# Kernel tuning notes

Measured on AMD Instinct MI355X. Metric: run time of the kernel, lower is better.

The kernel has to match this reference:

```python
import jax, jax.numpy as jnp
import numpy as np
import math

B, L, M, D, EL, H = 128, 105, 55, 256, 3, 1
PATCH = [3, 5, 7]

def pos_embed(T, d):
    pos = jnp.arange(T, dtype=jnp.float32)[:, None]
    div = jnp.exp(jnp.arange(0, d, 2, dtype=jnp.float32) * (-math.log(10000.0) / d))
    pe = jnp.zeros((T, d), dtype=jnp.float32)
    pe = pe.at[:, 0::2].set(jnp.sin(pos * div))
    pe = pe.at[:, 1::2].set(jnp.cos(pos * div))
    return pe

def circular_conv(x, w):
    # x: [N, T, Cin], w: [Dout, Cin, 3]; Conv1d kernel 3, circular padding 1, no bias
    xc = jnp.pad(x.transpose(0, 2, 1), ((0, 0), (0, 0), (1, 1)), mode='wrap')
    y = jax.lax.conv_general_dilated(xc, w, (1,), 'VALID', dimension_numbers=('NCH', 'OIH', 'NCH'))
    return y.transpose(0, 2, 1)

def _forward(x, conv_p0, conv_n0, conv_p1, conv_n1, conv_p2, conv_n2, Wq, bq, Wk, bk):
    convs = [(conv_p0, conv_n0), (conv_p1, conv_n1), (conv_p2, conv_n2)]
    # RevIN 'norm': per-sample standardization over time; stats are detached in torch
    mean = jax.lax.stop_gradient(jnp.mean(x, axis=1, keepdims=True))
    std = jax.lax.stop_gradient(jnp.sqrt(jnp.var(x, axis=1, keepdims=True) + 1e-5))
    xr = (x - mean) / std                      # [B, L, M]
    xt = xr.transpose(0, 2, 1)                 # [B, M, L]
    dk = D // H
    scale = 1.0 / math.sqrt(dk)
    series_list, prior_list = [], []
    for i, p in enumerate(PATCH):
        n = L // p
        # patch-size branch: (b m) n p -> embed over n with in_channels=p
        x_size = circular_conv(xt.reshape(B * M, n, p), convs[i][0]) + pos_embed(n, D)
        # patch-num branch: (b m) p n -> embed over p with in_channels=n
        x_num = circular_conv(xt.reshape(B * M, p, n), convs[i][1]) + pos_embed(p, D)
        for l in range(EL):
            def attn_mean(z):
                T = z.shape[1]
                q = (z @ Wq[l] + bq[l]).reshape(B * M, T, H, dk)
                k = (z @ Wk[l] + bk[l]).reshape(B * M, T, H, dk)
                a = jax.nn.softmax(scale * jnp.einsum('blhe,bshe->bhls', q, k), axis=-1)
                # fuse: mean over channel BEFORE expanding to window size
                # (repeat/tile commutes with the channel-mean, avoids [B*M,H,L,L])
                return a.reshape(B, M, H, T, T).mean(axis=1)   # [B, H, T, T]
            a_size = attn_mean(x_size)                          # [B, H, n, n]
            # einops repeat '(m rm) (n rn)': element-wise contiguous repeat
            series_list.append(jnp.repeat(jnp.repeat(a_size, p, axis=-2), p, axis=-1))
            a_num = attn_mean(x_num)                            # [B, H, p, p]
            # torch .repeat: tiling
            prior_list.append(jnp.tile(a_num, (1, 1, n, n)))
    # order: patch-major, layer-minor (matches the flattened lists)
    return jnp.stack(series_list), jnp.stack(prior_list)        # each [9, B, H, L, L]

def setup_inputs():
    key = jax.random.key(0)
    ks = jax.random.split(key, 12)
    s = 0.05
    inp = {"x": jax.random.normal(ks[0], (B, L, M), jnp.float32)}
    for i, p in enumerate(PATCH):
        inp[f"conv_p{i}"] = s * jax.random.normal(ks[1 + 2 * i], (D, p, 3), jnp.float32)
        inp[f"conv_n{i}"] = s * jax.random.normal(ks[2 + 2 * i], (D, L // p, 3), jnp.float32)
    inp["Wq"] = s * jax.random.normal(ks[7], (EL, D, D), jnp.float32)
    inp["bq"] = jnp.zeros((EL, D), jnp.float32)
    inp["Wk"] = s * jax.random.normal(ks[8], (EL, D, D), jnp.float32)
    inp["bk"] = jnp.zeros((EL, D), jnp.float32)
    return inp

def reference(x, conv_p0, conv_n0, conv_p1, conv_n1, conv_p2, conv_n2, Wq, bq, Wk, bk):
    return _forward(x, conv_p0, conv_n0, conv_p1, conv_n1, conv_p2, conv_n2, Wq, bq, Wk, bk)
```

## Files before the change

kernel.cpp:

```cpp
#include <hip/hip_runtime.h>
#include <hip/hip_bf16.h>

#define B_ 128
#define L_ 105
#define M_ 55
#define D_ 256
#define NCOMBO 18

#define WS_XT    0
#define WS_PE    739200
#define WS_LEFT  761216
#define WS_RIGHT 1258880
#define WS_MM    1756544
#define WS_MP    761216
#define WS_ACC   1258880
#define LR_STRIDE 27648
#define MM_STRIDE 11664
#define MP_STRIDE 12544
#define ACC_TOT  758016

#define WS_LRP        1966592
#define LRP_KZ_STRIDE 27648
#define LRP_C_STRIDE  110592
#define LRP_HALF      1990656
#define WS_NEED_BYTES ((size_t)(WS_LRP + 2 * LRP_HALF) * 4)

__constant__ int c_peOff[6] = {0, 35, 38, 59, 64, 79};
__constant__ int c_accbase[18] = {0,1225,2450, 3675,3684,3693, 3702,4143,4584,
                                  5025,5050,5075, 5100,5325,5550, 5775,5824,5873};

__device__ __forceinline__ void combo_dims(int c, int& i, int& br, int& l,
                                           int& p, int& n, int& Cin, int& T, int& J) {
    i = c / 6; br = (c % 6) / 3; l = c % 3;
    p = 3 + 2 * i;
    n = L_ / p;
    Cin = br ? n : p;
    T   = br ? p : n;
    J = 3 * Cin;
}

__device__ __forceinline__ float dot4(float4 a, float4 b) {
    return a.x * b.x + a.y * b.y + a.z * b.z + a.w * b.w;
}

__global__ void revin_kernel(const float* __restrict__ x, float* __restrict__ ws) {
    int bm = blockIdx.x; int b = bm / M_; int m = bm % M_;
    int tid = threadIdx.x;
    __shared__ float s1[128], s2[128];
    float v = 0.f;
    if (tid < L_) v = x[(b * L_ + tid) * M_ + m];
    s1[tid] = v; s2[tid] = v * v;
    __syncthreads();
    for (int off = 64; off > 0; off >>= 1) {
        if (tid < off) { s1[tid] += s1[tid + off]; s2[tid] += s2[tid + off]; }
        __syncthreads();
    }
    float mean = s1[0] * (1.f / L_);
    float var  = s2[0] * (1.f / L_) - mean * mean;
    float rstd = rsqrtf(var + 1e-5f);
    if (tid < L_) ws[WS_XT + bm * L_ + tid] = (v - mean) * rstd;
}

__global__ void pe_kernel(float* __restrict__ ws) {
    int bi = blockIdx.x;
    int i = bi / 2, br = bi % 2;
    int p = 3 + 2 * i, n = L_ / p;
    int T = br ? p : n;
    int d = threadIdx.x;
    float divv = expf(-(float)(d & ~1) * (logf(10000.f) / (float)D_));
    float* base = ws + WS_PE + c_peOff[bi] * D_;
    for (int t = 0; t < T; ++t) {
        float arg = (float)t * divv;
        base[t * D_ + d] = (d & 1) ? cosf(arg) : sinf(arg);
    }
}

__global__ __launch_bounds__(256) void lr2_kernel(
                          const float* __restrict__ w0, const float* __restrict__ w1,
                          const float* __restrict__ w2c, const float* __restrict__ w3,
                          const float* __restrict__ w4, const float* __restrict__ w5,
                          const float* __restrict__ Wq, const float* __restrict__ bq,
                          const float* __restrict__ Wk, const float* __restrict__ bk,
                          float* __restrict__ ws) {
    int c = blockIdx.x;
    int i, br, l, p, n, Cin, T, J; combo_dims(c, i, br, l, p, n, Cin, T, J);
    int Mdim = J + T;
    int r0 = blockIdx.y * 8;
    if (r0 >= Mdim) return;
    int kz = blockIdx.z;
    int d0 = kz * 64;
    int wi = i * 2 + br;
    const float* conv = (wi == 0) ? w0 : (wi == 1) ? w1 : (wi == 2) ? w2c
                       : (wi == 3) ? w3 : (wi == 4) ? w4 : w5;
    __shared__ float S[8][64];
    int tid = threadIdx.x;
    for (int idx = tid; idx < 8 * 64; idx += 256) {
        int rr = idx >> 6, dd = idx & 63;
        int row = r0 + rr; float val = 0.f;
        int d = d0 + dd;
        if (row < J) val = conv[d * J + row];
        else if (row < Mdim) val = ws[WS_PE + (c_peOff[wi] + (row - J)) * D_ + d];
        S[rr][dd] = val;
    }
    __syncthreads();
    const float* wqp = Wq + l * D_ * D_;
    const float* wkp = Wk + l * D_ * D_;
    float accL[8], accR[8];
#pragma unroll
    for (int rr = 0; rr < 8; ++rr) { accL[rr] = 0.f; accR[rr] = 0.f; }
    int o = tid;
#pragma unroll 8
    for (int dd = 0; dd < 64; ++dd) {
        int d = d0 + dd;
        float wqv = wqp[d * D_ + o];
        float wkv = wkp[d * D_ + o];
#pragma unroll
        for (int rr = 0; rr < 8; ++rr) {
            float sv = S[rr][dd];
            accL[rr] += sv * wqv;
            accR[rr] += sv * wkv;
        }
    }
    float bqv = (kz == 0) ? bq[l * D_ + o] : 0.f;
    float bkv = (kz == 0) ? bk[l * D_ + o] : 0.f;
    float* Lp = ws + WS_LRP + c * LRP_C_STRIDE + kz * LRP_KZ_STRIDE;
    float* Rp = Lp + LRP_HALF;
#pragma unroll
    for (int rr = 0; rr < 8; ++rr) {
        int row = r0 + rr;
        if (row < Mdim) {
            float aq = (row >= J) ? bqv : 0.f;
            float ak = (row >= J) ? bkv : 0.f;
            Lp[row * D_ + o] = accL[rr] + aq;
            Rp[row * D_ + o] = accR[rr] + ak;
        }
    }
}

__global__ __launch_bounds__(256) void lr_kernel(
                          const float* __restrict__ w0, const float* __restrict__ w1,
                          const float* __restrict__ w2c, const float* __restrict__ w3,
                          const float* __restrict__ w4, const float* __restrict__ w5,
                          const float* __restrict__ Wq, const float* __restrict__ bq,
                          const float* __restrict__ Wk, const float* __restrict__ bk,
                          float* __restrict__ ws) {
    int c = blockIdx.x;
    int i, br, l, p, n, Cin, T, J; combo_dims(c, i, br, l, p, n, Cin, T, J);
    int Mdim = J + T;
    int r0 = blockIdx.y * 4;
    if (r0 >= Mdim) return;
    int wi = i * 2 + br;
    const float* conv = (wi == 0) ? w0 : (wi == 1) ? w1 : (wi == 2) ? w2c
                       : (wi == 3) ? w3 : (wi == 4) ? w4 : w5;
    __shared__ float S[4][256];
    int tid = threadIdx.x;
    for (int idx = tid; idx < 4 * 256; idx += 256) {
        int rr = idx >> 8, dd = idx & 255;
        int row = r0 + rr; float val = 0.f;
        if (row < J) val = conv[dd * J + row];
        else if (row < Mdim) val = ws[WS_PE + (c_peOff[wi] + (row - J)) * D_ + dd];
        S[rr][dd] = val;
    }
    __syncthreads();
    const float* wqp = Wq + l * D_ * D_;
    const float* wkp = Wk + l * D_ * D_;
    float accL[4], accR[4];
#pragma unroll
    for (int rr = 0; rr < 4; ++rr) { accL[rr] = 0.f; accR[rr] = 0.f; }
    int o = tid;
#pragma unroll 8
    for (int d = 0; d < D_; ++d) {
        float wqv = wqp[d * D_ + o];
        float wkv = wkp[d * D_ + o];
#pragma unroll
        for (int rr = 0; rr < 4; ++rr) {
            float sv = S[rr][d];
            accL[rr] += sv * wqv;
            accR[rr] += sv * wkv;
        }
    }
    float bqv = bq[l * D_ + o], bkv = bk[l * D_ + o];
#pragma unroll
    for (int rr = 0; rr < 4; ++rr) {
        int row = r0 + rr;
        if (row < Mdim) {
            float aq = (row >= J) ? bqv : 0.f;
            float ak = (row >= J) ? bkv : 0.f;
            ws[WS_LEFT  + c * LR_STRIDE + row * D_ + o] = accL[rr] + aq;
            ws[WS_RIGHT + c * LR_STRIDE + row * D_ + o] = accR[rr] + ak;
        }
    }
}

__global__ void mm_kernel(float* __restrict__ ws, int use_partial) {
    int c = blockIdx.x;
    int i, br, l, p, n, Cin, T, J; combo_dims(c, i, br, l, p, n, Cin, T, J);
    int Mdim = J + T;
    int tr = blockIdx.y / 7, tc = blockIdx.y % 7;
    int r0 = tr * 16, c0 = tc * 16;
    if (r0 >= Mdim || c0 >= Mdim) return;
    __shared__ __align__(16) float Lb[16][260], Rb[16][260];
    int tid = threadIdx.x;
    if (use_partial) {
        const float* Lp = ws + WS_LRP + c * LRP_C_STRIDE;
        const float* Rp = Lp + LRP_HALF;
        for (int idx = tid; idx < 16 * 256; idx += 256) {
            int rr = idx >> 8, d = idx & 255;
            int rL = r0 + rr, rR = c0 + rr;
            float lv = 0.f, rv = 0.f;
            if (rL < Mdim) {
                int base = rL * D_ + d;
                lv = Lp[base] + Lp[base + LRP_KZ_STRIDE]
                   + Lp[base + 2 * LRP_KZ_STRIDE] + Lp[base + 3 * LRP_KZ_STRIDE];
            }
            if (rR < Mdim) {
                int base = rR * D_ + d;
                rv = Rp[base] + Rp[base + LRP_KZ_STRIDE]
                   + Rp[base + 2 * LRP_KZ_STRIDE] + Rp[base + 3 * LRP_KZ_STRIDE];
            }
            Lb[rr][d] = lv; Rb[rr][d] = rv;
        }
    } else {
        for (int idx = tid; idx < 16 * 256; idx += 256) {
            int rr = idx >> 8, d = idx & 255;
            int rL = r0 + rr, rR = c0 + rr;
            Lb[rr][d] = (rL < Mdim) ? ws[WS_LEFT  + c * LR_STRIDE + rL * D_ + d] : 0.f;
            Rb[rr][d] = (rR < Mdim) ? ws[WS_RIGHT + c * LR_STRIDE + rR * D_ + d] : 0.f;
        }
    }
    __syncthreads();
    int rr = tid / 16, cc = tid % 16;
    const float4* lrow = (const float4*)(&Lb[rr][0]);
    const float4* rrow = (const float4*)(&Rb[cc][0]);
    float acc = 0.f;
#pragma unroll 8
    for (int d4 = 0; d4 < 64; ++d4) {
        float4 a = lrow[d4], bb = rrow[d4];
        acc += a.x * bb.x + a.y * bb.y + a.z * bb.z + a.w * bb.w;
    }
    int r = r0 + rr, cth = c0 + cc;
    if (r < Mdim && cth < Mdim)
        ws[WS_MM + c * MM_STRIDE + r * Mdim + cth] = acc;
}

__global__ void pack_kernel(float* __restrict__ ws) {
    int c = blockIdx.x;
    int i, br, l, p, n, Cin, T, J; combo_dims(c, i, br, l, p, n, Cin, T, J);
    int Mdim = J + T;
    int Cinp = (Cin + 3) & ~3;
    int Jp = 3 * Cinp;
    int T4 = (T + 3) & ~3;
    int W = Jp + T4;
    const float* MMc = ws + WS_MM + c * MM_STRIDE;
    float* Mp = ws + WS_MP + c * MP_STRIDE;
    for (int e = threadIdx.x; e < W * W; e += 256) {
        int r = e / W, o = e % W;
        int srcr = -1, srcc = -1;
        bool brow = false;
        if (r < Jp) {
            int k = r / Cinp, cin = r % Cinp;
            if (cin < Cin) srcr = cin * 3 + k;
        } else {
            int t = r - Jp;
            if (t < T) { srcr = J + t; brow = true; }
        }
        if (o < Jp) {
            int k2 = o / Cinp, cin2 = o % Cinp;
            if (cin2 < Cin) srcc = cin2 * 3 + k2;
        } else {
            int s = o - Jp;
            if (s < T) srcc = J + s;
        }
        float val;
        if (srcr >= 0 && srcc >= 0) val = MMc[srcr * Mdim + srcc];
        else if (brow && o >= Jp && srcc < 0) val = -1e30f;
        else val = 0.f;
        Mp[e] = val;
    }
}

__global__ void zero_acc(float* __restrict__ ws) {
    int idx = blockIdx.x * 256 + threadIdx.x;
    if (idx < ACC_TOT / 4) {
        float4 z; z.x = 0.f; z.y = 0.f; z.z = 0.f; z.w = 0.f;
        ((float4*)(ws + WS_ACC))[idx] = z;
    }
}

template<int P, int BR>
__global__ __launch_bounds__(256) void attn2(const float* __restrict__ ws,
                                             float* __restrict__ wsw) {
    constexpr int N    = L_ / P;
    constexpr int Cin  = BR ? N : P;
    constexpr int T    = BR ? P : N;
    constexpr int Cinp = (Cin + 3) & ~3;
    constexpr int Jp   = 3 * Cinp;
    constexpr int T4   = (T + 3) & ~3;
    constexpr int W    = Jp + T4;
    constexpr int W4   = W / 4;
    constexpr int ST   = T4 + 1;
    constexpr int II   = (P - 3) / 2;
    constexpr int MC   = BR ? (P == 3 ? 12 : 8) : (P == 7 ? 8 : 4);
    constexpr int NT   = (MC / 4) * T * W4;
    constexpr int TPB  = (NT + 255) / 256;
    constexpr int MCQ  = MC / 4;
    constexpr int CQ   = Cinp / 4;
    constexpr int S4N  = T4 / 4;
    constexpr int OFF_X2T = 0;
    constexpr int OFF_X2A = OFF_X2T + T * Cinp * MC;
    constexpr int OFF_MSL = OFF_X2A + T * Cinp * MC;
    constexpr int OFF_G   = OFF_MSL + Cinp * W;
    constexpr int OFF_S   = OFF_G + MC * T * W;
    constexpr int TOT     = OFF_S + MC * T * ST;
    static_assert(TOT * 4 <= 65536, "LDS budget");

    __shared__ __align__(16) float smem[TOT];
    const int tid = threadIdx.x;
    const int b = blockIdx.x, l = blockIdx.y, sp = blockIdx.z;
    const int c = II * 6 + BR * 3 + l;
    const int m0 = sp * MC;
    const int vm = (M_ - m0 < MC) ? (M_ - m0) : MC;

    const float*  Mpg  = ws + WS_MP + c * MP_STRIDE;
    const float4* Mpg4 = (const float4*)Mpg;

    for (int e = tid; e < T * Cinp * MC; e += 256) {
        int mcol = e % MC, rest = e / MC;
        int cin = rest % Cinp, trow = rest / Cinp;
        float v = 0.f;
        if (cin < Cin && m0 + mcol < M_)
            v = ws[WS_XT + (size_t)(b * M_ + m0 + mcol) * L_ + trow * Cin + cin];
        smem[OFF_X2T + e] = v;
    }
    for (int e = tid; e < T * Cinp * MC; e += 256) {
        int cin = e % Cinp, trow = (e / Cinp) % T, mcol = e / (Cinp * T);
        float v = 0.f;
        if (cin < Cin && m0 + mcol < M_)
            v = ws[WS_XT + (size_t)(b * M_ + m0 + mcol) * L_ + trow * Cin + cin];
        smem[OFF_X2A + e] = v;
    }

    const float4* X2T4 = (const float4*)(smem + OFF_X2T);
    const float4* X2A4 = (const float4*)(smem + OFF_X2A);
    float4*       MSL4 = (float4*)(smem + OFF_MSL);
    float4*       G4w  = (float4*)(smem + OFF_G);
    const float4* G4   = (const float4*)(smem + OFF_G);

    float a[TPB][4][4];
#pragma unroll
    for (int tt = 0; tt < TPB; ++tt) {
        int q = tid + tt * 256;
        if (q < NT) {
            int o4 = q % W4, t = (q / W4) % T;
            float4 bv = Mpg4[(Jp + t) * W4 + o4];
#pragma unroll
            for (int am = 0; am < 4; ++am) {
                a[tt][am][0] = bv.x; a[tt][am][1] = bv.y;
                a[tt][am][2] = bv.z; a[tt][am][3] = bv.w;
            }
        }
    }
    __syncthreads();
    for (int k = 0; k < 3; ++k) {
        for (int e = tid; e < Cinp * W4; e += 256)
            MSL4[e] = Mpg4[k * Cinp * W4 + e];
        __syncthreads();
#pragma unroll
        for (int tt = 0; tt < TPB; ++tt) {
            int q = tid + tt * 256;
            if (q < NT) {
                int o4 = q % W4, t = (q / W4) % T, m4 = q / (W4 * T);
                int trow = t + k - 1;
                if (trow < 0) trow += T;
                if (trow >= T) trow -= T;
                const float4* xp = X2T4 + trow * Cinp * MCQ + m4;
                const float4* mp = MSL4 + o4;
#pragma unroll 4
                for (int cin = 0; cin < Cinp; ++cin) {
                    float4 x4 = xp[cin * MCQ];
                    float4 mv = mp[cin * W4];
#pragma unroll
                    for (int aq = 0; aq < 4; ++aq) {
                        float m = (aq == 0) ? mv.x : (aq == 1) ? mv.y : (aq == 2) ? mv.z : mv.w;
                        a[tt][0][aq] += x4.x * m;
                        a[tt][1][aq] += x4.y * m;
                        a[tt][2][aq] += x4.z * m;
                        a[tt][3][aq] += x4.w * m;
                    }
                }
            }
        }
        __syncthreads();
    }
#pragma unroll
    for (int tt = 0; tt < TPB; ++tt) {
        int q = tid + tt * 256;
        if (q < NT) {
            int o4 = q % W4, t = (q / W4) % T, m4 = q / (W4 * T);
#pragma unroll
            for (int am = 0; am < 4; ++am) {
                float4 o;
                o.x = a[tt][am][0]; o.y = a[tt][am][1];
                o.z = a[tt][am][2]; o.w = a[tt][am][3];
                G4w[((m4 * 4 + am) * T + t) * W4 + o4] = o;
            }
        }
    }
    __syncthreads();

    for (int it = tid; it < MC * T * S4N; it += 256) {
        int s4 = it % S4N, t = (it / S4N) % T, mc = it / (S4N * T);
        float acc[4];
#pragma unroll
        for (int q = 0; q < 4; ++q)
            acc[q] = smem[OFF_G + (mc * T + t) * W + Jp + s4 * 4 + q];
        for (int j4 = 0; j4 < Jp / 4; ++j4) {
            int k = j4 / CQ, cinq = j4 % CQ;
            float4 g = G4[(mc * T + t) * W4 + j4];
#pragma unroll
            for (int q = 0; q < 4; ++q) {
                int s = s4 * 4 + q;
                int trow = s + k - 1;
                if (trow < 0) trow += T;
                if (trow >= T) trow -= T;
                float4 x4 = X2A4[(mc * T + trow) * CQ + cinq];
                acc[q] += g.x * x4.x + g.y * x4.y + g.z * x4.z + g.w * x4.w;
            }
        }
#pragma unroll
        for (int q = 0; q < 4; ++q)
            smem[OFF_S + (mc * T + t) * ST + s4 * 4 + q] = 0.0625f * acc[q];
    }
    __syncthreads();

    for (int rid = tid; rid < MC * T; rid += 256) {
        int base = OFF_S + rid * ST;
        float pr[T4];
#pragma unroll
        for (int s = 0; s < T4; ++s) pr[s] = smem[base + s];
        float mx = -1e30f;
#pragma unroll
        for (int s = 0; s < T4; ++s) mx = fmaxf(mx, pr[s]);
        float sum = 0.f;
#pragma unroll
        for (int s = 0; s < T4; ++s) { pr[s] = __expf(pr[s] - mx); sum += pr[s]; }
        float inv = 1.f / sum;
#pragma unroll
        for (int s = 0; s < T; ++s) smem[base + s] = pr[s] * inv;
    }
    __syncthreads();

    float* accp = wsw + WS_ACC + c_accbase[c] * 128 + b * T * T;
    for (int e = tid; e < T * T; e += 256) {
        int t = e / T, s = e % T;
        float v = 0.f;
        for (int mc = 0; mc < vm; ++mc)
            v += smem[OFF_S + (mc * T + t) * ST + s];
        atomicAdd(&accp[e], v);
    }
}

template<int P, int BR>
__device__ __forceinline__ void expand_body(const float* __restrict__ acc,
                                            float* __restrict__ outp) {
    constexpr int T = BR ? P : (L_ / P);
    for (int idx = threadIdx.x; idx < L_ * L_; idx += 256) {
        int r = idx / L_, c2 = idx % L_;
        int rt = BR ? (r % P) : (r / P);
        int ct = BR ? (c2 % P) : (c2 / P);
        outp[idx] = acc[rt * T + ct];
    }
}

__global__ __launch_bounds__(256) void expand_kernel(const float* __restrict__ ws,
                                                     float* __restrict__ out) {
    int c = blockIdx.x, b = blockIdx.y;
    int i = c / 6, br = (c % 6) / 3, l = c % 3;
    int p = 3 + 2 * i;
    int T = br ? p : (L_ / p);
    __shared__ float sAcc[1232];
    int abase = c_accbase[c] * 128 + b * T * T;
    for (int idx = threadIdx.x; idx < T * T; idx += 256)
        sAcc[idx] = ws[WS_ACC + abase + idx] * (1.f / (float)M_);
    __syncthreads();
    float* outp = out + ((size_t)(br * 9 + i * 3 + l) * B_ + (size_t)b) * (size_t)(L_ * L_);
    int key = i * 2 + br;
    switch (key) {
        case 0: expand_body<3, 0>(sAcc, outp); break;
        case 1: expand_body<3, 1>(sAcc, outp); break;
        case 2: expand_body<5, 0>(sAcc, outp); break;
        case 3: expand_body<5, 1>(sAcc, outp); break;
        case 4: expand_body<7, 0>(sAcc, outp); break;
        case 5: expand_body<7, 1>(sAcc, outp); break;
    }
}

extern "C" void kernel_launch(void* const* d_in, const int* in_sizes, int n_in,
                              void* d_out, int out_size, void* d_ws, size_t ws_size,
                              hipStream_t stream) {
    const float* x   = (const float*)d_in[0];
    const float* cp0 = (const float*)d_in[1];
    const float* cn0 = (const float*)d_in[2];
    const float* cp1 = (const float*)d_in[3];
    const float* cn1 = (const float*)d_in[4];
    const float* cp2 = (const float*)d_in[5];
    const float* cn2 = (const float*)d_in[6];
    const float* Wq  = (const float*)d_in[7];
    const float* bq  = (const float*)d_in[8];
    const float* Wk  = (const float*)d_in[9];
    const float* bk  = (const float*)d_in[10];
    float* ws = (float*)d_ws;
    float* out = (float*)d_out;

    const int use_partial = (ws_size >= WS_NEED_BYTES) ? 1 : 0;

    hipLaunchKernelGGL(revin_kernel, dim3(B_ * M_), dim3(128), 0, stream, x, ws);
    hipLaunchKernelGGL(pe_kernel, dim3(6), dim3(256), 0, stream, ws);
    if (use_partial) {
        hipLaunchKernelGGL(lr2_kernel, dim3(NCOMBO, 14, 4), dim3(256), 0, stream,
                           cp0, cn0, cp1, cn1, cp2, cn2, Wq, bq, Wk, bk, ws);
    } else {
        hipLaunchKernelGGL(lr_kernel, dim3(NCOMBO, 27), dim3(256), 0, stream,
                           cp0, cn0, cp1, cn1, cp2, cn2, Wq, bq, Wk, bk, ws);
    }
    hipLaunchKernelGGL(mm_kernel, dim3(NCOMBO, 49), dim3(256), 0, stream, ws, use_partial);
    hipLaunchKernelGGL(pack_kernel, dim3(NCOMBO), dim3(256), 0, stream, ws);
    hipLaunchKernelGGL(zero_acc, dim3((ACC_TOT / 4 + 255) / 256), dim3(256), 0, stream, ws);

    hipLaunchKernelGGL((attn2<3, 0>), dim3(B_, 3, 14), dim3(256), 0, stream, ws, ws);
    hipLaunchKernelGGL((attn2<3, 1>), dim3(B_, 3, 5),  dim3(256), 0, stream, ws, ws);
    hipLaunchKernelGGL((attn2<5, 0>), dim3(B_, 3, 14), dim3(256), 0, stream, ws, ws);
    hipLaunchKernelGGL((attn2<5, 1>), dim3(B_, 3, 7),  dim3(256), 0, stream, ws, ws);
    hipLaunchKernelGGL((attn2<7, 0>), dim3(B_, 3, 7),  dim3(256), 0, stream, ws, ws);
    hipLaunchKernelGGL((attn2<7, 1>), dim3(B_, 3, 7),  dim3(256), 0, stream, ws, ws);

    hipLaunchKernelGGL(expand_kernel, dim3(NCOMBO, B_), dim3(256), 0, stream, ws, out);
}
```

Measured before the change: 484.1 us.

## Split query rows across two blocks in patch-size-3 attention kernel

For the P=3 patch-size branch (T=35), each block now handles only half the query rows. The grid z-dimension doubles and results for each half are accumulated atomically. This cuts per-thread register accumulators and LDS use per block and raises parallelism for the largest attention case. The cost is that each half-block reloads the full X and M slices, and there are twice as many blocks and atomics.

```diff
diff --git a/kernel.cpp b/kernel.cpp
--- a/kernel.cpp
+++ b/kernel.cpp
@@ -301,7 +301,9 @@
     constexpr int ST   = T4 + 1;
     constexpr int II   = (P - 3) / 2;
     constexpr int MC   = BR ? (P == 3 ? 12 : 8) : (P == 7 ? 8 : 4);
-    constexpr int NT   = (MC / 4) * T * W4;
+    constexpr int TH   = (BR == 0 && P == 3) ? 2 : 1;
+    constexpr int TSUB = (T + TH - 1) / TH;
+    constexpr int NT   = (MC / 4) * TSUB * W4;
     constexpr int TPB  = (NT + 255) / 256;
     constexpr int MCQ  = MC / 4;
     constexpr int CQ   = Cinp / 4;
@@ -310,13 +312,17 @@
     constexpr int OFF_X2A = OFF_X2T + T * Cinp * MC;
     constexpr int OFF_MSL = OFF_X2A + T * Cinp * MC;
     constexpr int OFF_G   = OFF_MSL + Cinp * W;
-    constexpr int OFF_S   = OFF_G + MC * T * W;
-    constexpr int TOT     = OFF_S + MC * T * ST;
+    constexpr int OFF_S   = OFF_G + MC * TSUB * W;
+    constexpr int TOT     = OFF_S + MC * TSUB * ST;
     static_assert(TOT * 4 <= 65536, "LDS budget");
 
     __shared__ __align__(16) float smem[TOT];
     const int tid = threadIdx.x;
-    const int b = blockIdx.x, l = blockIdx.y, sp = blockIdx.z;
+    const int b = blockIdx.x, l = blockIdx.y;
+    const int sp = blockIdx.z / TH;
+    const int th = blockIdx.z % TH;
+    const int t0 = th * TSUB;
+    const int TC = (T - t0 < TSUB) ? (T - t0) : TSUB;
     const int c = II * 6 + BR * 3 + l;
     const int m0 = sp * MC;
     const int vm = (M_ - m0 < MC) ? (M_ - m0) : MC;
@@ -351,12 +357,14 @@
     for (int tt = 0; tt < TPB; ++tt) {
         int q = tid + tt * 256;
         if (q < NT) {
-            int o4 = q % W4, t = (q / W4) % T;
-            float4 bv = Mpg4[(Jp + t) * W4 + o4];
-#pragma unroll
-            for (int am = 0; am < 4; ++am) {
-                a[tt][am][0] = bv.x; a[tt][am][1] = bv.y;
-                a[tt][am][2] = bv.z; a[tt][am][3] = bv.w;
+            int o4 = q % W4, tl = (q / W4) % TSUB;
+            if (tl < TC) {
+                float4 bv = Mpg4[(Jp + t0 + tl) * W4 + o4];
+#pragma unroll
+                for (int am = 0; am < 4; ++am) {
+                    a[tt][am][0] = bv.x; a[tt][am][1] = bv.y;
+                    a[tt][am][2] = bv.z; a[tt][am][3] = bv.w;
+                }
             }
         }
     }
@@ -369,23 +377,26 @@
         for (int tt = 0; tt < TPB; ++tt) {
             int q = tid + tt * 256;
             if (q < NT) {
-                int o4 = q % W4, t = (q / W4) % T, m4 = q / (W4 * T);
-                int trow = t + k - 1;
-                if (trow < 0) trow += T;
-                if (trow >= T) trow -= T;
-                const float4* xp = X2T4 + trow * Cinp * MCQ + m4;
-                const float4* mp = MSL4 + o4;
+                int o4 = q % W4, tl = (q / W4) % TSUB, m4 = q / (W4 * TSUB);
+                if (tl < TC) {
+                    int trow = t0 + tl + k - 1;
+                    if (trow < 0) trow += T;
+                    if (trow >= T) trow -= T;
+                    const float4* xp = X2T4 + trow * Cinp * MCQ + m4;
+                    const float4* mp = MSL4 + o4;
 #pragma unroll 4
-                for (int cin = 0; cin < Cinp; ++cin) {
-                    float4 x4 = xp[cin * MCQ];
-                    float4 mv = mp[cin * W4];
-#pragma unroll
-                    for (int aq = 0; aq < 4; ++aq) {
-                        float m = (aq == 0) ? mv.x : (aq == 1) ? mv.y : (aq == 2) ? mv.z : mv.w;
-                        a[tt][0][aq] += x4.x * m;
-                        a[tt][1][aq] += x4.y * m;
-                        a[tt][2][aq] += x4.z * m;
-                        a[tt][3][aq] += x4.w * m;
+                    for (int cin = 0; cin < Cinp; ++cin) {
+                        float4 x4 = xp[cin * MCQ];
+                        float4 mv = mp[cin * W4];
+#pragma unroll
+                        for (int aq = 0; aq < 4; ++aq) {
+                            float m = (aq == 0) ? mv.x : (aq == 1) ? mv.y
+                                    : (aq == 2) ? mv.z : mv.w;
+                            a[tt][0][aq] += x4.x * m;
+                            a[tt][1][aq] += x4.y * m;
+                            a[tt][2][aq] += x4.z * m;
+                            a[tt][3][aq] += x4.w * m;
+                        }
                     }
                 }
             }
@@ -396,27 +407,29 @@
     for (int tt = 0; tt < TPB; ++tt) {
         int q = tid + tt * 256;
         if (q < NT) {
-            int o4 = q % W4, t = (q / W4) % T, m4 = q / (W4 * T);
-#pragma unroll
-            for (int am = 0; am < 4; ++am) {
-                float4 o;
-                o.x = a[tt][am][0]; o.y = a[tt][am][1];
-                o.z = a[tt][am][2]; o.w = a[tt][am][3];
-                G4w[((m4 * 4 + am) * T + t) * W4 + o4] = o;
+            int o4 = q % W4, tl = (q / W4) % TSUB, m4 = q / (W4 * TSUB);
+            if (tl < TC) {
+#pragma unroll
+                for (int am = 0; am < 4; ++am) {
+                    float4 o;
+                    o.x = a[tt][am][0]; o.y = a[tt][am][1];
+                    o.z = a[tt][am][2]; o.w = a[tt][am][3];
+                    G4w[((m4 * 4 + am) * TSUB + tl) * W4 + o4] = o;
+                }
             }
         }
     }
     __syncthreads();
 
-    for (int it = tid; it < MC * T * S4N; it += 256) {
-        int s4 = it % S4N, t = (it / S4N) % T, mc = it / (S4N * T);
+    for (int it = tid; it < MC * TC * S4N; it += 256) {
+        int s4 = it % S4N, tl = (it / S4N) % TC, mc = it / (S4N * TC);
         float acc[4];
 #pragma unroll
         for (int q = 0; q < 4; ++q)
-            acc[q] = smem[OFF_G + (mc * T + t) * W + Jp + s4 * 4 + q];
+            acc[q] = smem[OFF_G + (mc * TSUB + tl) * W + Jp + s4 * 4 + q];
         for (int j4 = 0; j4 < Jp / 4; ++j4) {
             int k = j4 / CQ, cinq = j4 % CQ;
-            float4 g = G4[(mc * T + t) * W4 + j4];
+            float4 g = G4[(mc * TSUB + tl) * W4 + j4];
 #pragma unroll
             for (int q = 0; q < 4; ++q) {
                 int s = s4 * 4 + q;
@@ -429,12 +442,13 @@
         }
 #pragma unroll
         for (int q = 0; q < 4; ++q)
-            smem[OFF_S + (mc * T + t) * ST + s4 * 4 + q] = 0.0625f * acc[q];
-    }
-    __syncthreads();
-
-    for (int rid = tid; rid < MC * T; rid += 256) {
-        int base = OFF_S + rid * ST;
+            smem[OFF_S + (mc * TSUB + tl) * ST + s4 * 4 + q] = 0.0625f * acc[q];
+    }
+    __syncthreads();
+
+    for (int rid = tid; rid < MC * TC; rid += 256) {
+        int mc = rid / TC, tl = rid % TC;
+        int base = OFF_S + (mc * TSUB + tl) * ST;
         float pr[T4];
 #pragma unroll
         for (int s = 0; s < T4; ++s) pr[s] = smem[base + s];
@@ -451,12 +465,12 @@
     __syncthreads();
 
     float* accp = wsw + WS_ACC + c_accbase[c] * 128 + b * T * T;
-    for (int e = tid; e < T * T; e += 256) {
-        int t = e / T, s = e % T;
+    for (int e = tid; e < TC * T; e += 256) {
+        int tl = e / T, s = e % T;
         float v = 0.f;
         for (int mc = 0; mc < vm; ++mc)
-            v += smem[OFF_S + (mc * T + t) * ST + s];
-        atomicAdd(&accp[e], v);
+            v += smem[OFF_S + (mc * TSUB + tl) * ST + s];
+        atomicAdd(&accp[(t0 + tl) * T + s], v);
     }
 }
 
@@ -527,7 +541,7 @@
     hipLaunchKernelGGL(pack_kernel, dim3(NCOMBO), dim3(256), 0, stream, ws);
     hipLaunchKernelGGL(zero_acc, dim3((ACC_TOT / 4 + 255) / 256), dim3(256), 0, stream, ws);
 
-    hipLaunchKernelGGL((attn2<3, 0>), dim3(B_, 3, 14), dim3(256), 0, stream, ws, ws);
+    hipLaunchKernelGGL((attn2<3, 0>), dim3(B_, 3, 28), dim3(256), 0, stream, ws, ws);
     hipLaunchKernelGGL((attn2<3, 1>), dim3(B_, 3, 5),  dim3(256), 0, stream, ws, ws);
     hipLaunchKernelGGL((attn2<5, 0>), dim3(B_, 3, 14), dim3(256), 0, stream, ws, ws);
     hipLaunchKernelGGL((attn2<5, 1>), dim3(B_, 3, 7),  dim3(256), 0, stream, ws, ws);
```

Measured after the change: 482.5 us. Within noise of the previous version (-0.3%).

## Add specialized register-tiled attention kernel for patch-size branch

Applied to the files above, without the earlier changes.

Adds a new attnP kernel for the patch-size branches (BR=0) that computes the score stage with 4x4 register tiles over (t, s), reading from a row-permuted G buffer and a reordered copy of X so the float4 loads do not collide in LDS. The three BR=0 launches now use this kernel, while the attn2 MC selection is simplified to apply only to BR=1. The new kernel aims to cut LDS traffic and increase arithmetic intensity in the second contraction. In exchange it uses more shared memory and more registers per thread, which may lower occupancy.

```diff
diff --git a/kernel.cpp b/kernel.cpp
--- a/kernel.cpp
+++ b/kernel.cpp
@@ -287,6 +287,203 @@
     }
 }
 
+template<int P>
+__global__ __launch_bounds__(256) void attnP(const float* __restrict__ ws,
+                                             float* __restrict__ wsw) {
+    constexpr int T    = L_ / P;
+    constexpr int Cin  = P;
+    constexpr int Cinp = (Cin + 3) & ~3;
+    constexpr int CQ   = Cinp / 4;
+    constexpr int Jp   = 3 * Cinp;
+    constexpr int J4   = Jp / 4;
+    constexpr int T4   = (T + 3) & ~3;
+    constexpr int S4N  = T4 / 4;
+    constexpr int TQ4  = T4 / 4;
+    constexpr int W    = Jp + T4;
+    constexpr int W4   = W / 4;
+    constexpr int W4S  = W4 | 1;
+    constexpr int ST   = T4 + 1;
+    constexpr int MC   = (P == 7) ? 8 : 4;
+    constexpr int MCQ  = MC / 4;
+    constexpr int II   = (P - 3) / 2;
+    constexpr int RQ   = (T + 3) / 4;
+    constexpr int RPAD = 4 * RQ;
+    constexpr int NT   = (MC / 4) * T * W4;
+    constexpr int TPB  = (NT + 255) / 256;
+    constexpr int OFF_X2T = 0;
+    constexpr int OFF_XA  = OFF_X2T + T * Cinp * MC;
+    constexpr int OFF_MSL = OFF_XA + MC * RPAD * Cinp;
+    constexpr int OFF_G   = OFF_MSL + Cinp * W;
+    constexpr int OFF_S   = OFF_G + MC * T4 * W4S * 4;
+    constexpr int TOT     = OFF_S + MC * T4 * ST;
+    static_assert(TOT * 4 <= 65536, "LDS budget");
+
+    __shared__ __align__(16) float smem[TOT];
+    const int tid = threadIdx.x;
+    const int b = blockIdx.x, l = blockIdx.y, sp = blockIdx.z;
+    const int c = II * 6 + l;
+    const int m0 = sp * MC;
+    const int vm = (M_ - m0 < MC) ? (M_ - m0) : MC;
+
+    const float*  Mpg  = ws + WS_MP + c * MP_STRIDE;
+    const float4* Mpg4 = (const float4*)Mpg;
+
+    for (int e = tid; e < T * Cinp * MC; e += 256) {
+        int mcol = e % MC, rest = e / MC;
+        int cin = rest % Cinp, trow = rest / Cinp;
+        float v = 0.f;
+        if (cin < Cin && m0 + mcol < M_)
+            v = ws[WS_XT + (size_t)(b * M_ + m0 + mcol) * L_ + trow * Cin + cin];
+        smem[OFF_X2T + e] = v;
+    }
+    for (int e = tid; e < MC * RPAD * Cinp; e += 256) {
+        int cin = e % Cinp;
+        int rp  = (e / Cinp) % RPAD;
+        int mc  = e / (Cinp * RPAD);
+        int aa = rp / RQ, bb = rp % RQ;
+        int trow = bb * 4 + aa;
+        float v = 0.f;
+        if (cin < Cin && trow < T && m0 + mc < M_)
+            v = ws[WS_XT + (size_t)(b * M_ + m0 + mc) * L_ + trow * Cin + cin];
+        smem[OFF_XA + e] = v;
+    }
+
+    const float4* X2T4 = (const float4*)(smem + OFF_X2T);
+    const float4* XA4  = (const float4*)(smem + OFF_XA);
+    float4*       MSL4 = (float4*)(smem + OFF_MSL);
+    float4*       G4w  = (float4*)(smem + OFF_G);
+    const float4* G4   = (const float4*)(smem + OFF_G);
+
+    float a[TPB][4][4];
+#pragma unroll
+    for (int tt = 0; tt < TPB; ++tt) {
+        int q = tid + tt * 256;
+        if (q < NT) {
+            int o4 = q % W4, t = (q / W4) % T;
+            float4 bv = Mpg4[(Jp + t) * W4 + o4];
+#pragma unroll
+            for (int am = 0; am < 4; ++am) {
+                a[tt][am][0] = bv.x; a[tt][am][1] = bv.y;
+                a[tt][am][2] = bv.z; a[tt][am][3] = bv.w;
+            }
+        }
+    }
+    __syncthreads();
+    for (int k = 0; k < 3; ++k) {
+        for (int e = tid; e < Cinp * W4; e += 256)
+            MSL4[e] = Mpg4[k * Cinp * W4 + e];
+        __syncthreads();
+#pragma unroll
+        for (int tt = 0; tt < TPB; ++tt) {
+            int q = tid + tt * 256;
+            if (q < NT) {
+                int o4 = q % W4, t = (q / W4) % T, m4 = q / (W4 * T);
+                int trow = t + k - 1;
+                if (trow < 0) trow += T;
+                if (trow >= T) trow -= T;
+                const float4* xp = X2T4 + trow * Cinp * MCQ + m4;
+                const float4* mp = MSL4 + o4;
+#pragma unroll 4
+                for (int cin = 0; cin < Cinp; ++cin) {
+                    float4 x4 = xp[cin * MCQ];
+                    float4 mv = mp[cin * W4];
+#pragma unroll
+                    for (int aq = 0; aq < 4; ++aq) {
+                        float m = (aq == 0) ? mv.x : (aq == 1) ? mv.y
+                                : (aq == 2) ? mv.z : mv.w;
+                        a[tt][0][aq] += x4.x * m;
+                        a[tt][1][aq] += x4.y * m;
+                        a[tt][2][aq] += x4.z * m;
+                        a[tt][3][aq] += x4.w * m;
+                    }
+                }
+            }
+        }
+        __syncthreads();
+    }
+#pragma unroll
+    for (int tt = 0; tt < TPB; ++tt) {
+        int q = tid + tt * 256;
+        if (q < NT) {
+            int o4 = q % W4, t = (q / W4) % T, m4 = q / (W4 * T);
+#pragma unroll
+            for (int am = 0; am < 4; ++am) {
+                int rowp = (t & 3) * (MC * TQ4) + (m4 * 4 + am) * TQ4 + (t >> 2);
+                float4 o;
+                o.x = a[tt][am][0]; o.y = a[tt][am][1];
+                o.z = a[tt][am][2]; o.w = a[tt][am][3];
+                G4w[rowp * W4S + o4] = o;
+            }
+        }
+    }
+    __syncthreads();
+
+    for (int it = tid; it < MC * TQ4 * S4N; it += 256) {
+        int s4 = it % S4N, tq = (it / S4N) % TQ4, mc = it / (S4N * TQ4);
+        float acc[4][4];
+#pragma unroll
+        for (int at = 0; at < 4; ++at) {
+            float4 e = G4[((at * MC + mc) * TQ4 + tq) * W4S + J4 + s4];
+            acc[at][0] = e.x; acc[at][1] = e.y; acc[at][2] = e.z; acc[at][3] = e.w;
+        }
+#pragma unroll
+        for (int j4 = 0; j4 < J4; ++j4) {
+            int k = j4 / CQ, cinq = j4 % CQ;
+            float4 g[4];
+#pragma unroll
+            for (int at = 0; at < 4; ++at)
+                g[at] = G4[((at * MC + mc) * TQ4 + tq) * W4S + j4];
+#pragma unroll
+            for (int q = 0; q < 4; ++q) {
+                int s = s4 * 4 + q;
+                int trow = s + k - 1;
+                if (trow < 0) trow += T;
+                if (trow >= T) trow -= T;
+                float4 x4 = XA4[mc * (RPAD * CQ) + (trow & 3) * (RQ * CQ)
+                                + (trow >> 2) * CQ + cinq];
+#pragma unroll
+                for (int at = 0; at < 4; ++at)
+                    acc[at][q] += dot4(g[at], x4);
+            }
+        }
+#pragma unroll
+        for (int at = 0; at < 4; ++at) {
+            int t = tq * 4 + at;
+#pragma unroll
+            for (int q = 0; q < 4; ++q)
+                smem[OFF_S + (mc * T4 + t) * ST + s4 * 4 + q] = 0.0625f * acc[at][q];
+        }
+    }
+    __syncthreads();
+
+    for (int rid = tid; rid < MC * T; rid += 256) {
+        int mc = rid / T, tl = rid % T;
+        int base = OFF_S + (mc * T4 + tl) * ST;
+        float pr[T4];
+#pragma unroll
+        for (int s = 0; s < T4; ++s) pr[s] = smem[base + s];
+        float mx = -1e30f;
+#pragma unroll
+        for (int s = 0; s < T4; ++s) mx = fmaxf(mx, pr[s]);
+        float sum = 0.f;
+#pragma unroll
+        for (int s = 0; s < T4; ++s) { pr[s] = __expf(pr[s] - mx); sum += pr[s]; }
+        float inv = 1.f / sum;
+#pragma unroll
+        for (int s = 0; s < T; ++s) smem[base + s] = pr[s] * inv;
+    }
+    __syncthreads();
+
+    float* accp = wsw + WS_ACC + c_accbase[c] * 128 + b * T * T;
+    for (int e = tid; e < T * T; e += 256) {
+        int t = e / T, s = e % T;
+        float v = 0.f;
+        for (int mc = 0; mc < vm; ++mc)
+            v += smem[OFF_S + (mc * T4 + t) * ST + s];
+        atomicAdd(&accp[e], v);
+    }
+}
+
 template<int P, int BR>
 __global__ __launch_bounds__(256) void attn2(const float* __restrict__ ws,
                                              float* __restrict__ wsw) {
@@ -300,7 +497,7 @@
     constexpr int W4   = W / 4;
     constexpr int ST   = T4 + 1;
     constexpr int II   = (P - 3) / 2;
-    constexpr int MC   = BR ? (P == 3 ? 12 : 8) : (P == 7 ? 8 : 4);
+    constexpr int MC   = P == 3 ? 12 : 8;
     constexpr int NT   = (MC / 4) * T * W4;
     constexpr int TPB  = (NT + 255) / 256;
     constexpr int MCQ  = MC / 4;
@@ -381,7 +578,8 @@
                     float4 mv = mp[cin * W4];
 #pragma unroll
                     for (int aq = 0; aq < 4; ++aq) {
-                        float m = (aq == 0) ? mv.x : (aq == 1) ? mv.y : (aq == 2) ? mv.z : mv.w;
+                        float m = (aq == 0) ? mv.x : (aq == 1) ? mv.y
+                                : (aq == 2) ? mv.z : mv.w;
                         a[tt][0][aq] += x4.x * m;
                         a[tt][1][aq] += x4.y * m;
                         a[tt][2][aq] += x4.z * m;
@@ -527,11 +725,11 @@
     hipLaunchKernelGGL(pack_kernel, dim3(NCOMBO), dim3(256), 0, stream, ws);
     hipLaunchKernelGGL(zero_acc, dim3((ACC_TOT / 4 + 255) / 256), dim3(256), 0, stream, ws);
 
-    hipLaunchKernelGGL((attn2<3, 0>), dim3(B_, 3, 14), dim3(256), 0, stream, ws, ws);
+    hipLaunchKernelGGL((attnP<3>),    dim3(B_, 3, 14), dim3(256), 0, stream, ws, ws);
     hipLaunchKernelGGL((attn2<3, 1>), dim3(B_, 3, 5),  dim3(256), 0, stream, ws, ws);
-    hipLaunchKernelGGL((attn2<5, 0>), dim3(B_, 3, 14), dim3(256), 0, stream, ws, ws);
+    hipLaunchKernelGGL((attnP<5>),    dim3(B_, 3, 14), dim3(256), 0, stream, ws, ws);
     hipLaunchKernelGGL((attn2<5, 1>), dim3(B_, 3, 7),  dim3(256), 0, stream, ws, ws);
-    hipLaunchKernelGGL((attn2<7, 0>), dim3(B_, 3, 7),  dim3(256), 0, stream, ws, ws);
+    hipLaunchKernelGGL((attnP<7>),    dim3(B_, 3, 7),  dim3(256), 0, stream, ws, ws);
     hipLaunchKernelGGL((attn2<7, 1>), dim3(B_, 3, 7),  dim3(256), 0, stream, ws, ws);
 
     hipLaunchKernelGGL(expand_kernel, dim3(NCOMBO, B_), dim3(256), 0, stream, ws, out);
```

Result: slower. 513.5 us (+6.1%).
